# Kernel optimization log

Measured on AMD Instinct MI355X. Metric: run time of the kernel, lower is better.

The kernel has to match this reference:

```python
import jax, jax.numpy as jnp
import numpy as np

D_MODEL = 1024
N_HEADS = 16
HEAD_DIM = D_MODEL // N_HEADS
ROPE_BASE = 10000.0


def setup_inputs() -> dict:
    key = jax.random.key(0)
    ks = jax.random.split(key, 5)
    B, S = 2, 2048
    x = jax.random.normal(ks[0], (B, S, D_MODEL), dtype=jnp.float32)
    scale = 1.0 / np.sqrt(D_MODEL)
    Wq = jax.random.normal(ks[1], (D_MODEL, D_MODEL), dtype=jnp.float32) * scale
    Wk = jax.random.normal(ks[2], (D_MODEL, D_MODEL), dtype=jnp.float32) * scale
    Wv = jax.random.normal(ks[3], (D_MODEL, D_MODEL), dtype=jnp.float32) * scale
    Wo = jax.random.normal(ks[4], (D_MODEL, D_MODEL), dtype=jnp.float32) * scale
    return {"x": x, "Wq": Wq, "Wk": Wk, "Wv": Wv, "Wo": Wo}


def _rope_cos_sin(seq_len, dtype):
    # inv_freq over half the head dim, duplicated (cat[freqs, freqs])
    inv_freq = 1.0 / (ROPE_BASE ** (jnp.arange(0, HEAD_DIM, 2, dtype=jnp.float32) / HEAD_DIM))
    t = jnp.arange(seq_len, dtype=jnp.float32)
    freqs = jnp.outer(t, inv_freq)                 # [S, HD/2]
    emb = jnp.concatenate([freqs, freqs], axis=-1)  # [S, HD]
    return jnp.cos(emb).astype(dtype), jnp.sin(emb).astype(dtype)


def _rotate_half(v):
    v1, v2 = jnp.split(v, 2, axis=-1)
    return jnp.concatenate([-v2, v1], axis=-1)


def reference(x, Wq, Wk, Wv, Wo):
    B, S, _ = x.shape
    # torch Linear: y = x @ W.T  (weights stored [out, in])
    def proj(W):
        y = jnp.einsum('bsd,ed->bse', x, W)
        return y.reshape(B, S, N_HEADS, HEAD_DIM).transpose(0, 2, 1, 3)  # [B,H,S,HD]
    q, k, v = proj(Wq), proj(Wk), proj(Wv)

    cos, sin = _rope_cos_sin(S, x.dtype)  # [S, HD]
    cos = cos[None, None]                 # [1,1,S,HD]
    sin = sin[None, None]
    q = q * cos + _rotate_half(q) * sin
    k = k * cos + _rotate_half(k) * sin

    scale = 1.0 / np.sqrt(HEAD_DIM)
    scores = jnp.einsum('bhqd,bhkd->bhqk', q, k) * scale  # [B,H,S,S]
    causal = jnp.triu(jnp.ones((S, S), dtype=bool), k=1)
    scores = jnp.where(causal, jnp.finfo(scores.dtype).min, scores)
    attn = jax.nn.softmax(scores, axis=-1)
    out = jnp.einsum('bhqk,bhkd->bhqd', attn, v)          # [B,H,S,HD]
    out = out.transpose(0, 2, 1, 3).reshape(B, S, D_MODEL)
    return jnp.einsum('bsd,ed->bse', out, Wo)
```

## Files before the change

kernel.cpp:

```cpp
#include <hip/hip_runtime.h>

typedef unsigned short u16;
typedef __attribute__((ext_vector_type(8))) short short8;
typedef __attribute__((ext_vector_type(4))) float floatx4;

#define D_MODEL 1024
#define NHEADS 16
#define HD 64
#define BATCH 2
#define SEQ 2048
#define MROWS (BATCH * SEQ)

static __device__ __forceinline__ u16 f2bf(float f) {
  unsigned int u = __float_as_uint(f);
  u += 0x7fffu + ((u >> 16) & 1u);
  return (u16)(u >> 16);
}

__global__ void cvt_all(const float* __restrict__ x, const float* __restrict__ wq,
                        const float* __restrict__ wk, const float* __restrict__ wv,
                        const float* __restrict__ wo, u16* __restrict__ xb,
                        u16* __restrict__ wqkvb, u16* __restrict__ wob) {
  const int i = blockIdx.x * 256 + threadIdx.x;
  const int chunk = i >> 18;
  const float* src;
  u16* dst;
  int loc;
  switch (chunk) {
    case 0: case 1: case 2: case 3: src = x;  dst = xb;              loc = i;              break;
    case 4:                          src = wq; dst = wqkvb;           loc = i - (4 << 18); break;
    case 5:                          src = wk; dst = wqkvb + 1048576; loc = i - (5 << 18); break;
    case 6:                          src = wv; dst = wqkvb + 2097152; loc = i - (6 << 18); break;
    default:                         src = wo; dst = wob;             loc = i - (7 << 18); break;
  }
  const float4 v = ((const float4*)src)[loc];
  ushort4 o;
  o.x = f2bf(v.x); o.y = f2bf(v.y); o.z = f2bf(v.z); o.w = f2bf(v.w);
  ((ushort4*)dst)[loc] = o;
}

__global__ __launch_bounds__(256) void gemm_qkv(
    const u16* __restrict__ A, const u16* __restrict__ B,
    u16* __restrict__ qb, u16* __restrict__ kb, u16* __restrict__ vb, int K) {
  __shared__ u16 As[128 * 32];
  __shared__ u16 Bs[128 * 32];
  const int t = threadIdx.x;
  const int lane = t & 63;
  const int wv = t >> 6;
  const int wr = wv >> 1, wc = wv & 1;
  const int m0 = blockIdx.y * 128, n0 = blockIdx.x * 128;
  const int qd = lane >> 4, lr = lane & 15;
  const int arow = lane >> 2;
  const int acol = (lane & 3) * 8;

  floatx4 acc[4][4];
#pragma unroll
  for (int i = 0; i < 4; ++i)
#pragma unroll
    for (int j = 0; j < 4; ++j) acc[i][j] = (floatx4){0.f, 0.f, 0.f, 0.f};

  for (int kt = 0; kt < K; kt += 32) {
    __syncthreads();
#pragma unroll
    for (int i = 0; i < 2; ++i) {
      const int seg = wv * 2 + i;
      const u16* ga = &A[(size_t)(m0 + seg * 16 + arow) * K + kt + acol];
      const u16* gb = &B[(size_t)(n0 + seg * 16 + arow) * K + kt + acol];
      __builtin_amdgcn_global_load_lds(
          (const __attribute__((address_space(1))) void*)ga,
          (__attribute__((address_space(3))) void*)&As[seg * 512], 16, 0, 0);
      __builtin_amdgcn_global_load_lds(
          (const __attribute__((address_space(1))) void*)gb,
          (__attribute__((address_space(3))) void*)&Bs[seg * 512], 16, 0, 0);
    }
    __syncthreads();

    short8 af[4], bfr[4];
#pragma unroll
    for (int i = 0; i < 4; ++i)
      af[i] = *(const short8*)&As[(wr * 64 + i * 16 + lr) * 32 + qd * 8];
#pragma unroll
    for (int j = 0; j < 4; ++j)
      bfr[j] = *(const short8*)&Bs[(wc * 64 + j * 16 + lr) * 32 + qd * 8];
#pragma unroll
    for (int i = 0; i < 4; ++i)
#pragma unroll
      for (int j = 0; j < 4; ++j)
        acc[i][j] = __builtin_amdgcn_mfma_f32_16x16x32_bf16(af[i], bfr[j], acc[i][j], 0, 0, 0);
  }

  const int tn = n0 >> 10;
  if (tn == 2) {
#pragma unroll
    for (int i = 0; i < 4; ++i) {
      const int mb = m0 + wr * 64 + i * 16 + qd * 4;
      const int b = mb >> 11, s = mb & 2047;
#pragma unroll
      for (int j = 0; j < 4; ++j) {
        const int nn = (n0 + wc * 64 + j * 16 + lr) & 1023;
        const int h = nn >> 6, d = nn & 63;
        ushort4 o;
        o.x = f2bf(acc[i][j][0]); o.y = f2bf(acc[i][j][1]);
        o.z = f2bf(acc[i][j][2]); o.w = f2bf(acc[i][j][3]);
        *(ushort4*)&vb[((size_t)(b * NHEADS + h) * HD + d) * SEQ + s] = o;
      }
    }
  } else {
    u16* dst = (tn == 0) ? qb : kb;
    const float qs = (tn == 0) ? 0.18033688011112042f : 1.0f;
    const int h = ((n0 & 1023) >> 6) + wc;
    const float inv0 = __builtin_exp2f(-(float)lr * 0.4152410118609203f);
    const float inv1 = __builtin_exp2f(-(float)(lr + 16) * 0.4152410118609203f);
#pragma unroll
    for (int i = 0; i < 4; ++i) {
      const int mb = m0 + wr * 64 + i * 16 + qd * 4;
      const int b = mb >> 11;
      const size_t rowbase = (size_t)(b * NHEADS + h) * SEQ;
#pragma unroll
      for (int r = 0; r < 4; ++r) {
        const int sq = (mb + r) & 2047;
        float s0, c0, s1, c1;
        __sincosf((float)sq * inv0, &s0, &c0);
        __sincosf((float)sq * inv1, &s1, &c1);
#pragma unroll
        for (int j = 0; j < 4; ++j) {
          const float v = acc[i][j][r];
          const float pv = acc[i][j ^ 2][r];
          const float cc = (j & 1) ? c1 : c0;
          const float ss = (j & 1) ? s1 : s0;
          const float res = (v * cc + ((j < 2) ? -pv : pv) * ss) * qs;
          dst[(rowbase + sq) * HD + j * 16 + lr] = f2bf(res);
        }
      }
    }
  }
}

__global__ __launch_bounds__(256) void gemm_out(
    const u16* __restrict__ A, const u16* __restrict__ B, float* __restrict__ fo,
    int N, int K) {
  __shared__ u16 As[64 * 32];
  __shared__ u16 Bs[128 * 32];
  const int t = threadIdx.x;
  const int lane = t & 63, wv = t >> 6;
  const int m0 = blockIdx.y * 64, n0 = blockIdx.x * 128;
  const int qd = lane >> 4, lr = lane & 15;
  const int arow = lane >> 2;
  const int acol = (lane & 3) * 8;

  floatx4 acc[8];
#pragma unroll
  for (int j = 0; j < 8; ++j) acc[j] = (floatx4){0.f, 0.f, 0.f, 0.f};

  for (int kt = 0; kt < K; kt += 32) {
    __syncthreads();
    {
      const u16* ga = &A[(size_t)(m0 + wv * 16 + arow) * K + kt + acol];
      __builtin_amdgcn_global_load_lds(
          (const __attribute__((address_space(1))) void*)ga,
          (__attribute__((address_space(3))) void*)&As[wv * 512], 16, 0, 0);
#pragma unroll
      for (int i = 0; i < 2; ++i) {
        const int seg = wv * 2 + i;
        const u16* gb = &B[(size_t)(n0 + seg * 16 + arow) * K + kt + acol];
        __builtin_amdgcn_global_load_lds(
            (const __attribute__((address_space(1))) void*)gb,
            (__attribute__((address_space(3))) void*)&Bs[seg * 512], 16, 0, 0);
      }
    }
    __syncthreads();
    const short8 af = *(const short8*)&As[(wv * 16 + lr) * 32 + qd * 8];
#pragma unroll
    for (int j = 0; j < 8; ++j) {
      const short8 bfr = *(const short8*)&Bs[(j * 16 + lr) * 32 + qd * 8];
      acc[j] = __builtin_amdgcn_mfma_f32_16x16x32_bf16(af, bfr, acc[j], 0, 0, 0);
    }
  }
#pragma unroll
  for (int j = 0; j < 8; ++j)
#pragma unroll
    for (int r = 0; r < 4; ++r)
      fo[(size_t)(m0 + wv * 16 + qd * 4 + r) * N + n0 + j * 16 + lr] = acc[j][r];
}

__global__ __launch_bounds__(128, 2) void flash_mfma(
    const u16* __restrict__ Q, const u16* __restrict__ Kg,
    const u16* __restrict__ Vg, u16* __restrict__ O) {
  __shared__ u16 Ks[2][2][64 * 32];
  __shared__ u16 Vs[2][2][64 * 32];
  __shared__ u16 Ps[2][16][72];
  const int t = threadIdx.x;
  const int lane = t & 63, wv = t >> 6;
  const int lr = lane & 15, qd = lane >> 4;
  const int bh = blockIdx.x;
  const int c = 15 - (int)blockIdx.y;
  const int nsteps = 2 * c + 2;
  const int q0w = c * 128 + wv * 64;
  const size_t baseQK = (size_t)bh * SEQ * HD;
  const size_t baseV = (size_t)bh * HD * SEQ;
  const int b = bh >> 4, h = bh & 15;
  const int srow = lane >> 2;
  const int scol = (lane & 3) * 8;

  auto stage = [&](int buf, int k0) {
    if (wv == 0) {
#pragma unroll
      for (int hh = 0; hh < 2; ++hh)
#pragma unroll
        for (int seg = 0; seg < 4; ++seg) {
          const u16* g = &Kg[baseQK + (size_t)(k0 + seg * 16 + srow) * HD + hh * 32 + scol];
          __builtin_amdgcn_global_load_lds(
              (const __attribute__((address_space(1))) void*)g,
              (__attribute__((address_space(3))) void*)&Ks[buf][hh][seg * 512], 16, 0, 0);
        }
    } else {
#pragma unroll
      for (int hh = 0; hh < 2; ++hh)
#pragma unroll
        for (int seg = 0; seg < 4; ++seg) {
          const u16* g = &Vg[baseV + (size_t)(seg * 16 + srow) * SEQ + k0 + hh * 32 + scol];
          __builtin_amdgcn_global_load_lds(
              (const __attribute__((address_space(1))) void*)g,
              (__attribute__((address_space(3))) void*)&Vs[buf][hh][seg * 512], 16, 0, 0);
        }
    }
  };

  short8 qf[4][2];
#pragma unroll
  for (int i = 0; i < 4; ++i)
#pragma unroll
    for (int s = 0; s < 2; ++s)
      qf[i][s] = *(const short8*)&Q[baseQK + (size_t)(q0w + i * 16 + lr) * HD + s * 32 + qd * 8];

  float l_i[4] = {0.f, 0.f, 0.f, 0.f};
  floatx4 oacc[4][4];
#pragma unroll
  for (int i = 0; i < 4; ++i)
#pragma unroll
    for (int dj = 0; dj < 4; ++dj) oacc[i][dj] = (floatx4){0.f, 0.f, 0.f, 0.f};

  stage(0, 0);

  for (int kt = 0; kt < nsteps; ++kt) {
    __syncthreads();
    if (kt + 1 < nsteps) stage((kt + 1) & 1, (kt + 1) * 64);
    const int k0 = kt * 64;
    if (k0 > q0w) continue;
    const int buf = kt & 1;

    short8 kf[2][4], vf[2][4];
#pragma unroll
    for (int s = 0; s < 2; ++s)
#pragma unroll
      for (int jj = 0; jj < 4; ++jj)
        kf[s][jj] = *(const short8*)&Ks[buf][s][(jj * 16 + lr) * 32 + qd * 8];
#pragma unroll
    for (int s = 0; s < 2; ++s)
#pragma unroll
      for (int dj = 0; dj < 4; ++dj)
        vf[s][dj] = *(const short8*)&Vs[buf][s][(dj * 16 + lr) * 32 + qd * 8];

    const bool diag = (k0 == q0w);
#pragma unroll
    for (int i = 0; i < 4; ++i) {
      floatx4 sv[4];
#pragma unroll
      for (int jj = 0; jj < 4; ++jj) sv[jj] = (floatx4){0.f, 0.f, 0.f, 0.f};
#pragma unroll
      for (int s = 0; s < 2; ++s)
#pragma unroll
        for (int jj = 0; jj < 4; ++jj)
          sv[jj] = __builtin_amdgcn_mfma_f32_16x16x32_bf16(kf[s][jj], qf[i][s], sv[jj], 0, 0, 0);

      if (diag) {
#pragma unroll
        for (int jj = 0; jj < 4; ++jj)
#pragma unroll
          for (int r = 0; r < 4; ++r)
            if (jj * 16 + qd * 4 + r > i * 16 + lr) sv[jj][r] = -1e30f;
      }

      float rs = 0.f;
#pragma unroll
      for (int jj = 0; jj < 4; ++jj) {
        const float p0 = __builtin_exp2f(sv[jj][0]);
        const float p1 = __builtin_exp2f(sv[jj][1]);
        const float p2 = __builtin_exp2f(sv[jj][2]);
        const float p3 = __builtin_exp2f(sv[jj][3]);
        rs += (p0 + p1) + (p2 + p3);
        uint2 pk;
        pk.x = __builtin_amdgcn_perm(__float_as_uint(p1), __float_as_uint(p0), 0x07060302);
        pk.y = __builtin_amdgcn_perm(__float_as_uint(p3), __float_as_uint(p2), 0x07060302);
        *(uint2*)&Ps[wv][lr][jj * 16 + qd * 4] = pk;
      }
      l_i[i] += rs;

      const short8 pf0 = *(const short8*)&Ps[wv][lr][qd * 8];
      const short8 pf1 = *(const short8*)&Ps[wv][lr][32 + qd * 8];
#pragma unroll
      for (int dj = 0; dj < 4; ++dj)
        oacc[i][dj] = __builtin_amdgcn_mfma_f32_16x16x32_bf16(pf0, vf[0][dj], oacc[i][dj], 0, 0, 0);
#pragma unroll
      for (int dj = 0; dj < 4; ++dj)
        oacc[i][dj] = __builtin_amdgcn_mfma_f32_16x16x32_bf16(pf1, vf[1][dj], oacc[i][dj], 0, 0, 0);
    }
  }

#pragma unroll
  for (int i = 0; i < 4; ++i) {
    float lf = l_i[i];
    lf += __shfl_xor(lf, 16, 64);
    lf += __shfl_xor(lf, 32, 64);
#pragma unroll
    for (int r = 0; r < 4; ++r) {
      const float linv = 1.f / __shfl(lf, qd * 4 + r, 64);
      const int q = q0w + i * 16 + qd * 4 + r;
#pragma unroll
      for (int dj = 0; dj < 4; ++dj)
        O[(size_t)(b * SEQ + q) * D_MODEL + h * HD + dj * 16 + lr] = f2bf(oacc[i][dj][r] * linv);
    }
  }
}

extern "C" void kernel_launch(void* const* d_in, const int* in_sizes, int n_in,
                              void* d_out, int out_size, void* d_ws, size_t ws_size,
                              hipStream_t stream) {
  const float* x  = (const float*)d_in[0];
  const float* Wq = (const float*)d_in[1];
  const float* Wk = (const float*)d_in[2];
  const float* Wv = (const float*)d_in[3];
  const float* Wo = (const float*)d_in[4];
  float* out = (float*)d_out;

  u16* xb = (u16*)d_ws;
  u16* wqkv = xb + 4194304;
  u16* wo = wqkv + 3145728;
  u16* qb = wo + 1048576;
  u16* kb = qb + 4194304;
  u16* vb = kb + 4194304;
  u16* ow = vb + 4194304;

  cvt_all<<<8192, 256, 0, stream>>>(x, Wq, Wk, Wv, Wo, xb, wqkv, wo);
  gemm_qkv<<<dim3(24, 32), 256, 0, stream>>>(xb, wqkv, qb, kb, vb, 1024);
  flash_mfma<<<dim3(32, 16), 128, 0, stream>>>(qb, kb, vb, ow);
  gemm_out<<<dim3(8, 64), 256, 0, stream>>>(ow, wo, out, 1024, 1024);
}
```

Before: 212.7 us.

## Split flash attention query tile across four waves of 32 rows

The flash attention block grows from 2 to 4 waves, each owning 32 query rows instead of 64. K/V staging is spread over all four waves, and the two row tiles' QK MFMAs are interleaved so they can issue back to back. Per-wave registers drop and there are more waves per CU to hide latency. The cost is that the same K/V tile is read from LDS by twice as many waves, and causal masking on the diagonal now uses per-row-tile offsets.

```diff
diff --git a/kernel.cpp b/kernel.cpp
--- a/kernel.cpp
+++ b/kernel.cpp
@@ -183,19 +183,19 @@
       fo[(size_t)(m0 + wv * 16 + qd * 4 + r) * N + n0 + j * 16 + lr] = acc[j][r];
 }
 
-__global__ __launch_bounds__(128, 2) void flash_mfma(
+__global__ __launch_bounds__(256, 2) void flash_mfma(
     const u16* __restrict__ Q, const u16* __restrict__ Kg,
     const u16* __restrict__ Vg, u16* __restrict__ O) {
   __shared__ u16 Ks[2][2][64 * 32];
   __shared__ u16 Vs[2][2][64 * 32];
-  __shared__ u16 Ps[2][16][72];
+  __shared__ u16 Ps[4][2][16][72];
   const int t = threadIdx.x;
   const int lane = t & 63, wv = t >> 6;
   const int lr = lane & 15, qd = lane >> 4;
   const int bh = blockIdx.x;
   const int c = 15 - (int)blockIdx.y;
   const int nsteps = 2 * c + 2;
-  const int q0w = c * 128 + wv * 64;
+  const int q0w = c * 128 + wv * 32;
   const size_t baseQK = (size_t)bh * SEQ * HD;
   const size_t baseV = (size_t)bh * HD * SEQ;
   const int b = bh >> 4, h = bh & 15;
@@ -203,40 +203,37 @@
   const int scol = (lane & 3) * 8;
 
   auto stage = [&](int buf, int k0) {
-    if (wv == 0) {
-#pragma unroll
-      for (int hh = 0; hh < 2; ++hh)
-#pragma unroll
-        for (int seg = 0; seg < 4; ++seg) {
-          const u16* g = &Kg[baseQK + (size_t)(k0 + seg * 16 + srow) * HD + hh * 32 + scol];
-          __builtin_amdgcn_global_load_lds(
-              (const __attribute__((address_space(1))) void*)g,
-              (__attribute__((address_space(3))) void*)&Ks[buf][hh][seg * 512], 16, 0, 0);
-        }
+    const int hh = wv & 1;
+    if (wv < 2) {
+#pragma unroll
+      for (int seg = 0; seg < 4; ++seg) {
+        const u16* g = &Kg[baseQK + (size_t)(k0 + seg * 16 + srow) * HD + hh * 32 + scol];
+        __builtin_amdgcn_global_load_lds(
+            (const __attribute__((address_space(1))) void*)g,
+            (__attribute__((address_space(3))) void*)&Ks[buf][hh][seg * 512], 16, 0, 0);
+      }
     } else {
 #pragma unroll
-      for (int hh = 0; hh < 2; ++hh)
-#pragma unroll
-        for (int seg = 0; seg < 4; ++seg) {
-          const u16* g = &Vg[baseV + (size_t)(seg * 16 + srow) * SEQ + k0 + hh * 32 + scol];
-          __builtin_amdgcn_global_load_lds(
-              (const __attribute__((address_space(1))) void*)g,
-              (__attribute__((address_space(3))) void*)&Vs[buf][hh][seg * 512], 16, 0, 0);
-        }
+      for (int seg = 0; seg < 4; ++seg) {
+        const u16* g = &Vg[baseV + (size_t)(seg * 16 + srow) * SEQ + k0 + hh * 32 + scol];
+        __builtin_amdgcn_global_load_lds(
+            (const __attribute__((address_space(1))) void*)g,
+            (__attribute__((address_space(3))) void*)&Vs[buf][hh][seg * 512], 16, 0, 0);
+      }
     }
   };
 
-  short8 qf[4][2];
-#pragma unroll
-  for (int i = 0; i < 4; ++i)
+  short8 qf[2][2];
+#pragma unroll
+  for (int i = 0; i < 2; ++i)
 #pragma unroll
     for (int s = 0; s < 2; ++s)
       qf[i][s] = *(const short8*)&Q[baseQK + (size_t)(q0w + i * 16 + lr) * HD + s * 32 + qd * 8];
 
-  float l_i[4] = {0.f, 0.f, 0.f, 0.f};
-  floatx4 oacc[4][4];
-#pragma unroll
-  for (int i = 0; i < 4; ++i)
+  float l_i[2] = {0.f, 0.f};
+  floatx4 oacc[2][4];
+#pragma unroll
+  for (int i = 0; i < 2; ++i)
 #pragma unroll
     for (int dj = 0; dj < 4; ++dj) oacc[i][dj] = (floatx4){0.f, 0.f, 0.f, 0.f};
 
@@ -246,7 +243,7 @@
     __syncthreads();
     if (kt + 1 < nsteps) stage((kt + 1) & 1, (kt + 1) * 64);
     const int k0 = kt * 64;
-    if (k0 > q0w) continue;
+    if (k0 > q0w + 31) continue;
     const int buf = kt & 1;
 
     short8 kf[2][4], vf[2][4];
@@ -261,43 +258,49 @@
       for (int dj = 0; dj < 4; ++dj)
         vf[s][dj] = *(const short8*)&Vs[buf][s][(dj * 16 + lr) * 32 + qd * 8];
 
-    const bool diag = (k0 == q0w);
-#pragma unroll
-    for (int i = 0; i < 4; ++i) {
-      floatx4 sv[4];
-#pragma unroll
-      for (int jj = 0; jj < 4; ++jj) sv[jj] = (floatx4){0.f, 0.f, 0.f, 0.f};
-#pragma unroll
-      for (int s = 0; s < 2; ++s)
+    floatx4 sv[2][4];
+#pragma unroll
+    for (int i = 0; i < 2; ++i)
+#pragma unroll
+      for (int jj = 0; jj < 4; ++jj) sv[i][jj] = (floatx4){0.f, 0.f, 0.f, 0.f};
+#pragma unroll
+    for (int s = 0; s < 2; ++s)
+#pragma unroll
+      for (int jj = 0; jj < 4; ++jj) {
+        sv[1][jj] = __builtin_amdgcn_mfma_f32_16x16x32_bf16(kf[s][jj], qf[1][s], sv[1][jj], 0, 0, 0);
+        sv[0][jj] = __builtin_amdgcn_mfma_f32_16x16x32_bf16(kf[s][jj], qf[0][s], sv[0][jj], 0, 0, 0);
+      }
+
+#pragma unroll
+    for (int i = 0; i < 2; ++i) {
+      const int dq = (q0w + i * 16) - k0;
+      if (dq < 63) {
 #pragma unroll
         for (int jj = 0; jj < 4; ++jj)
-          sv[jj] = __builtin_amdgcn_mfma_f32_16x16x32_bf16(kf[s][jj], qf[i][s], sv[jj], 0, 0, 0);
-
-      if (diag) {
-#pragma unroll
-        for (int jj = 0; jj < 4; ++jj)
 #pragma unroll
           for (int r = 0; r < 4; ++r)
-            if (jj * 16 + qd * 4 + r > i * 16 + lr) sv[jj][r] = -1e30f;
-      }
-
+            if (jj * 16 + qd * 4 + r > dq + lr) sv[i][jj][r] = -1e30f;
+      }
       float rs = 0.f;
 #pragma unroll
       for (int jj = 0; jj < 4; ++jj) {
-        const float p0 = __builtin_exp2f(sv[jj][0]);
-        const float p1 = __builtin_exp2f(sv[jj][1]);
-        const float p2 = __builtin_exp2f(sv[jj][2]);
-        const float p3 = __builtin_exp2f(sv[jj][3]);
+        const float p0 = __builtin_exp2f(sv[i][jj][0]);
+        const float p1 = __builtin_exp2f(sv[i][jj][1]);
+        const float p2 = __builtin_exp2f(sv[i][jj][2]);
+        const float p3 = __builtin_exp2f(sv[i][jj][3]);
         rs += (p0 + p1) + (p2 + p3);
         uint2 pk;
         pk.x = __builtin_amdgcn_perm(__float_as_uint(p1), __float_as_uint(p0), 0x07060302);
         pk.y = __builtin_amdgcn_perm(__float_as_uint(p3), __float_as_uint(p2), 0x07060302);
-        *(uint2*)&Ps[wv][lr][jj * 16 + qd * 4] = pk;
+        *(uint2*)&Ps[wv][i][lr][jj * 16 + qd * 4] = pk;
       }
       l_i[i] += rs;
-
-      const short8 pf0 = *(const short8*)&Ps[wv][lr][qd * 8];
-      const short8 pf1 = *(const short8*)&Ps[wv][lr][32 + qd * 8];
+    }
+
+#pragma unroll
+    for (int i = 0; i < 2; ++i) {
+      const short8 pf0 = *(const short8*)&Ps[wv][i][lr][qd * 8];
+      const short8 pf1 = *(const short8*)&Ps[wv][i][lr][32 + qd * 8];
 #pragma unroll
       for (int dj = 0; dj < 4; ++dj)
         oacc[i][dj] = __builtin_amdgcn_mfma_f32_16x16x32_bf16(pf0, vf[0][dj], oacc[i][dj], 0, 0, 0);
@@ -308,7 +311,7 @@
   }
 
 #pragma unroll
-  for (int i = 0; i < 4; ++i) {
+  for (int i = 0; i < 2; ++i) {
     float lf = l_i[i];
     lf += __shfl_xor(lf, 16, 64);
     lf += __shfl_xor(lf, 32, 64);
@@ -343,6 +346,6 @@
 
   cvt_all<<<8192, 256, 0, stream>>>(x, Wq, Wk, Wv, Wo, xb, wqkv, wo);
   gemm_qkv<<<dim3(24, 32), 256, 0, stream>>>(xb, wqkv, qb, kb, vb, 1024);
-  flash_mfma<<<dim3(32, 16), 128, 0, stream>>>(qb, kb, vb, ow);
+  flash_mfma<<<dim3(32, 16), 256, 0, stream>>>(qb, kb, vb, ow);
   gemm_out<<<dim3(8, 64), 256, 0, stream>>>(ow, wo, out, 1024, 1024);
 }
```

Measured after the change: 187.8 us. 11.7% less time.
